# Optimization experiments

Hardware: AMD Instinct MI355X
Metric: run time of the kernel (lower is better)

The kernel has to match this reference:

```python
import jax, jax.numpy as jnp
import numpy as np

N = 50000
F_IN = 128
HID = 16
CLS = 40
NEG_SLOPE = 0.2


def gat_layer(x, src, dst, W, a_src, a_dst, b, heads, out_ch):
    # x: [N, Fin]; src/dst: [E] (self-loops included); W: [Fin, heads*out_ch]
    n = x.shape[0]
    h = (x @ W).reshape(n, heads, out_ch)                    # [N, H, C]
    al_s = jnp.einsum('nhc,hc->nh', h, a_src)                # [N, H]
    al_d = jnp.einsum('nhc,hc->nh', h, a_dst)                # [N, H]
    e = jax.nn.leaky_relu(al_s[src] + al_d[dst], NEG_SLOPE)  # [E, H]
    # segment softmax over incoming edges of each dst node
    m = jax.ops.segment_max(e, dst, num_segments=n)          # [N, H]
    ex = jnp.exp(e - m[dst])
    den = jax.ops.segment_sum(ex, dst, num_segments=n)
    alpha = ex / den[dst]                                    # [E, H]
    out = jax.ops.segment_sum(h[src] * alpha[:, :, None], dst, num_segments=n)
    return out.reshape(n, heads * out_ch) + b


def setup_inputs() -> dict:
    key = jax.random.key(0)
    ks = jax.random.split(key, 16)
    E = 800000
    x = jax.random.normal(ks[0], (N, F_IN), dtype=jnp.float32)
    edge_index = jax.random.randint(ks[1], (2, E), 0, N, dtype=jnp.int64)
    s = 0.1
    W1 = jax.random.normal(ks[2], (F_IN, 7 * HID), dtype=jnp.float32) * s
    a_src1 = jax.random.normal(ks[3], (7, HID), dtype=jnp.float32) * s
    a_dst1 = jax.random.normal(ks[4], (7, HID), dtype=jnp.float32) * s
    b1 = jnp.zeros((7 * HID,), dtype=jnp.float32)
    W2 = jax.random.normal(ks[5], (7 * HID, 6 * HID), dtype=jnp.float32) * s
    a_src2 = jax.random.normal(ks[6], (6, HID), dtype=jnp.float32) * s
    a_dst2 = jax.random.normal(ks[7], (6, HID), dtype=jnp.float32) * s
    b2 = jnp.zeros((6 * HID,), dtype=jnp.float32)
    W3 = jax.random.normal(ks[8], (6 * HID, 6 * CLS), dtype=jnp.float32) * s
    a_src3 = jax.random.normal(ks[9], (6, CLS), dtype=jnp.float32) * s
    a_dst3 = jax.random.normal(ks[10], (6, CLS), dtype=jnp.float32) * s
    b3 = jnp.zeros((6 * CLS,), dtype=jnp.float32)
    return {
        'x': x, 'edge_index': edge_index,
        'W1': W1, 'a_src1': a_src1, 'a_dst1': a_dst1, 'b1': b1,
        'W2': W2, 'a_src2': a_src2, 'a_dst2': a_dst2, 'b2': b2,
        'W3': W3, 'a_src3': a_src3, 'a_dst3': a_dst3, 'b3': b3,
    }


def reference(x, edge_index, W1, a_src1, a_dst1, b1, W2, a_src2, a_dst2, b2, W3, a_src3, a_dst3, b3):
    # add self-loops once (PyG GATConv default add_self_loops=True)
    loops = jnp.arange(N, dtype=edge_index.dtype)
    src = jnp.concatenate([edge_index[0], loops])
    dst = jnp.concatenate([edge_index[1], loops])
    # dropout layers are identity in eval mode
    h = gat_layer(x, src, dst, W1, a_src1, a_dst1, b1, 7, HID)
    h = jax.nn.relu(h)
    h = gat_layer(h, src, dst, W2, a_src2, a_dst2, b2, 6, HID)
    h = jax.nn.relu(h)
    out = gat_layer(h, src, dst, W3, a_src3, a_dst3, b3, 6, CLS)
    return out
```

## Files before the change

### kernel.cpp

```cpp
#include <hip/hip_runtime.h>
#include <hip/hip_fp16.h>
#include <cstdint>

#define NNODES 50000

__device__ inline void wave_lds_fence() {
  asm volatile("s_waitcnt lgkmcnt(0)" ::: "memory");
  __builtin_amdgcn_wave_barrier();
}

__global__ void hist_kernel(const int* __restrict__ ei, int E, int Nn, int* __restrict__ cnt) {
  int i = blockIdx.x * blockDim.x + threadIdx.x;
  int ET = E + Nn;
  if (i >= ET) return;
  int d = (i < E) ? ei[E + i] : (i - E);
  atomicAdd(&cnt[d], 1);
}

__global__ void scan1_kernel(const int* __restrict__ in, int n, int* __restrict__ incl,
                             int* __restrict__ bsum) {
  __shared__ int sd[256];
  int g = blockIdx.x * 256 + threadIdx.x;
  int v = (g < n) ? in[g] : 0;
  sd[threadIdx.x] = v;
  __syncthreads();
  for (int off = 1; off < 256; off <<= 1) {
    int t = (threadIdx.x >= off) ? sd[threadIdx.x - off] : 0;
    __syncthreads();
    sd[threadIdx.x] += t;
    __syncthreads();
  }
  if (g < n) incl[g] = sd[threadIdx.x];
  if (threadIdx.x == 255) bsum[blockIdx.x] = sd[255];
}

__global__ void scan3_kernel(const int* __restrict__ incl, const int* __restrict__ bscan,
                             int n, int* __restrict__ rowptr) {
  int g = blockIdx.x * 256 + threadIdx.x;
  if (g == 0) rowptr[0] = 0;
  if (g < n) {
    int off = (blockIdx.x > 0) ? bscan[blockIdx.x - 1] : 0;
    rowptr[g + 1] = incl[g] + off;
  }
}

__global__ void scatter_kernel(const int* __restrict__ ei, int E, int Nn,
                               const int* __restrict__ rowptr, int* __restrict__ cnt2,
                               int* __restrict__ esorted) {
  int i = blockIdx.x * blockDim.x + threadIdx.x;
  int ET = E + Nn;
  if (i >= ET) return;
  int s, d;
  if (i < E) { s = ei[i]; d = ei[E + i]; }
  else       { s = i - E; d = i - E; }
  int pos = rowptr[d] + atomicAdd(&cnt2[d], 1);
  esorted[pos] = s;
}

template <int FIN, int HC, int HCP, int BLOCK>
__global__ __launch_bounds__(BLOCK) void gemm_kernel(const float* __restrict__ X,
                                                     const float* __restrict__ W,
                                                     __half* __restrict__ Hout) {
  constexpr int NT = 16;
  constexpr int TM = 4, TN = 4;
  constexpr int CG = HC / TN;
  __shared__ __align__(16) float xs[FIN * NT];
  const int n0 = blockIdx.x * NT;
  for (int i = threadIdx.x * 4; i < NT * FIN; i += BLOCK * 4) {
    float4 v = *(const float4*)(X + (size_t)n0 * FIN + i);
    int node = i / FIN, k = i % FIN;
    xs[(k + 0) * NT + node] = v.x;
    xs[(k + 1) * NT + node] = v.y;
    xs[(k + 2) * NT + node] = v.z;
    xs[(k + 3) * NT + node] = v.w;
  }
  __syncthreads();
  const int cg = threadIdx.x % CG;
  const int ng = threadIdx.x / CG;
  if (ng >= NT / TM) return;
  const int c0 = cg * TN;
  const int i0 = ng * TM;
  float acc[TM][TN];
#pragma unroll
  for (int i = 0; i < TM; ++i)
#pragma unroll
    for (int j = 0; j < TN; ++j) acc[i][j] = 0.f;
#pragma unroll 4
  for (int k = 0; k < FIN; ++k) {
    const float4 wv = *(const float4*)(W + (size_t)k * HC + c0);
    const float4 xv = *(const float4*)(xs + k * NT + i0);
    acc[0][0] += xv.x * wv.x; acc[0][1] += xv.x * wv.y; acc[0][2] += xv.x * wv.z; acc[0][3] += xv.x * wv.w;
    acc[1][0] += xv.y * wv.x; acc[1][1] += xv.y * wv.y; acc[1][2] += xv.y * wv.z; acc[1][3] += xv.y * wv.w;
    acc[2][0] += xv.z * wv.x; acc[2][1] += xv.z * wv.y; acc[2][2] += xv.z * wv.z; acc[2][3] += xv.z * wv.w;
    acc[3][0] += xv.w * wv.x; acc[3][1] += xv.w * wv.y; acc[3][2] += xv.w * wv.z; acc[3][3] += xv.w * wv.w;
  }
#pragma unroll
  for (int i = 0; i < TM; ++i) {
    union { __half2 h2[2]; uint2 u; } pk;
    pk.h2[0] = __floats2half2_rn(acc[i][0], acc[i][1]);
    pk.h2[1] = __floats2half2_rn(acc[i][2], acc[i][3]);
    *(uint2*)(Hout + (size_t)(n0 + i0 + i) * HCP + c0) = pk.u;
  }
}

template <int H, int C, int HCP>
__global__ void alpha_kernel(const __half* __restrict__ Hbuf, const float* __restrict__ a_s,
                             const float* __restrict__ a_d, float* __restrict__ als8,
                             float* __restrict__ ald8, int n_nodes) {
  int i = blockIdx.x * blockDim.x + threadIdx.x;
  if (i >= n_nodes * H) return;
  int n = i / H, h = i % H;
  const __half2* hp = (const __half2*)(Hbuf + (size_t)n * HCP + (size_t)h * C);
  float s1 = 0.f, s2 = 0.f;
#pragma unroll
  for (int c = 0; c < C / 2; ++c) {
    float2 f = __half22float2(hp[c]);
    s1 += f.x * a_s[h * C + 2 * c] + f.y * a_s[h * C + 2 * c + 1];
    s2 += f.x * a_d[h * C + 2 * c] + f.y * a_d[h * C + 2 * c + 1];
  }
  als8[n * 8 + h] = s1;
  ald8[n * 8 + h] = s2;
}

template <int H, int C, int HCP, int RELU>
__global__ __launch_bounds__(256) void agg_kernel(const __half* __restrict__ Hbuf,
                                                  const float* __restrict__ als8,
                                                  const float* __restrict__ ald8,
                                                  const int* __restrict__ rowptr,
                                                  const int* __restrict__ esrc,
                                                  const float* __restrict__ bias,
                                                  float* __restrict__ Out, int n_nodes) {
  constexpr int HC = H * C;
  constexpr int NCHUNK = HC / 8;
  constexpr int GROUPS = (NCHUNK <= 16) ? 4 : 2;
  constexpr int LPG = 64 / GROUPS;
  constexpr int UN = 3;
  constexpr int TPAD = 72;
  const int wave = threadIdx.x >> 6;
  const int lane = threadIdx.x & 63;
  const int grp = lane / LPG;
  const int lg = lane % LPG;
  const int n = blockIdx.x * 4 + wave;
  __shared__ float s_w[4][TPAD * H];
  __shared__ int s_src[4][TPAD];
  if (n >= n_nodes) return;

  if (lane < TPAD - 64) s_src[wave][64 + lane] = 0;
  for (int z = lane; z < (TPAD - 64) * H; z += 64) s_w[wave][64 * H + z] = 0.f;

  const int e0 = rowptr[n];
  const int e1 = rowptr[n + 1];

  float aldn[H];
#pragma unroll
  for (int h = 0; h < H; ++h) aldn[h] = ald8[n * 8 + h];

  const int head = min((lg * 8) / C, H - 1);
  const bool act = lg < NCHUNK;

  float acc[8];
  float lsum = 0.f;
#pragma unroll
  for (int j = 0; j < 8; ++j) acc[j] = 0.f;

  for (int base = e0; base < e1; base += 64) {
    const int cnt = (e1 - base < 64) ? (e1 - base) : 64;
    int sreg = 0;
    if (lane < cnt) sreg = esrc[base + lane];
    s_src[wave][lane] = sreg;
    if (lane < cnt) {
      const float4 qa = *(const float4*)(als8 + (size_t)sreg * 8);
      const float4 qb = *(const float4*)(als8 + (size_t)sreg * 8 + 4);
      const float q[8] = {qa.x, qa.y, qa.z, qa.w, qb.x, qb.y, qb.z, qb.w};
#pragma unroll
      for (int h = 0; h < H; ++h) {
        float v = q[h] + aldn[h];
        v = v > 0.f ? v : 0.2f * v;
        s_w[wave][lane * H + h] = __expf(v);
      }
    } else {
#pragma unroll
      for (int h = 0; h < H; ++h) s_w[wave][lane * H + h] = 0.f;
    }
    wave_lds_fence();
    const int nit = (cnt + GROUPS - 1) / GROUPS;
    for (int i = 0; i < nit; i += UN) {
      int tt[UN], si[UN];
      uint4 v[UN];
      float w[UN];
#pragma unroll
      for (int k = 0; k < UN; ++k) tt[k] = (i + k) * GROUPS + grp;
#pragma unroll
      for (int k = 0; k < UN; ++k) si[k] = s_src[wave][tt[k]];
#pragma unroll
      for (int k = 0; k < UN; ++k)
        if (act) v[k] = *(const uint4*)(Hbuf + (size_t)si[k] * HCP + lg * 8);
#pragma unroll
      for (int k = 0; k < UN; ++k) w[k] = s_w[wave][tt[k] * H + head];
#pragma unroll
      for (int k = 0; k < UN; ++k)
        if (act) {
          const __half2* hp = (const __half2*)&v[k];
          float2 f0 = __half22float2(hp[0]);
          float2 f1 = __half22float2(hp[1]);
          float2 f2 = __half22float2(hp[2]);
          float2 f3 = __half22float2(hp[3]);
          lsum += w[k];
          acc[0] += w[k] * f0.x; acc[1] += w[k] * f0.y;
          acc[2] += w[k] * f1.x; acc[3] += w[k] * f1.y;
          acc[4] += w[k] * f2.x; acc[5] += w[k] * f2.y;
          acc[6] += w[k] * f3.x; acc[7] += w[k] * f3.y;
        }
    }
    wave_lds_fence();
  }

#pragma unroll
  for (int off = LPG; off < 64; off <<= 1) {
    lsum += __shfl_xor(lsum, off);
#pragma unroll
    for (int j = 0; j < 8; ++j) acc[j] += __shfl_xor(acc[j], off);
  }

  if (grp == 0 && act) {
    const float inv = 1.f / lsum;
    const float4 b0 = *(const float4*)(bias + lg * 8);
    const float4 b1 = *(const float4*)(bias + lg * 8 + 4);
    float4 o0, o1;
    o0.x = acc[0] * inv + b0.x; o0.y = acc[1] * inv + b0.y;
    o0.z = acc[2] * inv + b0.z; o0.w = acc[3] * inv + b0.w;
    o1.x = acc[4] * inv + b1.x; o1.y = acc[5] * inv + b1.y;
    o1.z = acc[6] * inv + b1.z; o1.w = acc[7] * inv + b1.w;
    if (RELU) {
      o0.x = fmaxf(o0.x, 0.f); o0.y = fmaxf(o0.y, 0.f);
      o0.z = fmaxf(o0.z, 0.f); o0.w = fmaxf(o0.w, 0.f);
      o1.x = fmaxf(o1.x, 0.f); o1.y = fmaxf(o1.y, 0.f);
      o1.z = fmaxf(o1.z, 0.f); o1.w = fmaxf(o1.w, 0.f);
    }
    *(float4*)(Out + (size_t)n * HC + lg * 8) = o0;
    *(float4*)(Out + (size_t)n * HC + lg * 8 + 4) = o1;
  }
}

extern "C" void kernel_launch(void* const* d_in, const int* in_sizes, int n_in,
                              void* d_out, int out_size, void* d_ws, size_t ws_size,
                              hipStream_t stream) {
  const int N = NNODES;
  const float* x  = (const float*)d_in[0];
  const int* ei   = (const int*)d_in[1];
  const float* W1 = (const float*)d_in[2];
  const float* as1 = (const float*)d_in[3];
  const float* ad1 = (const float*)d_in[4];
  const float* b1  = (const float*)d_in[5];
  const float* W2  = (const float*)d_in[6];
  const float* as2 = (const float*)d_in[7];
  const float* ad2 = (const float*)d_in[8];
  const float* b2  = (const float*)d_in[9];
  const float* W3  = (const float*)d_in[10];
  const float* as3 = (const float*)d_in[11];
  const float* ad3 = (const float*)d_in[12];
  const float* b3  = (const float*)d_in[13];
  float* out = (float*)d_out;
  const int E = in_sizes[1] / 2;
  const int ET = E + N;

  char* ws = (char*)d_ws;
  size_t off = 0;
  auto alloc = [&](size_t bytes) -> char* {
    char* p = ws + off;
    off += (bytes + 255) & ~(size_t)255;
    return p;
  };
  int* cnt     = (int*)alloc((size_t)N * 4);
  int* cnt2    = (int*)alloc((size_t)N * 4);
  int* incl    = (int*)alloc((size_t)N * 4);
  int* bsum    = (int*)alloc(512 * 4);
  int* bscan   = (int*)alloc(256 * 4);
  int* rowptr  = (int*)alloc((size_t)(N + 1) * 4);
  int* esorted = (int*)alloc((size_t)ET * 4);
  float* als   = (float*)alloc((size_t)N * 8 * 4);
  float* ald   = (float*)alloc((size_t)N * 8 * 4);
  __half* hbuf = (__half*)alloc((size_t)N * 256 * 2);
  float* abuf  = (float*)alloc((size_t)N * 112 * 4);

  hipMemsetAsync(cnt, 0, (size_t)N * 4, stream);
  hipMemsetAsync(cnt2, 0, (size_t)N * 4, stream);

  const int B1 = (N + 255) / 256;
  hist_kernel<<<(ET + 255) / 256, 256, 0, stream>>>(ei, E, N, cnt);
  scan1_kernel<<<B1, 256, 0, stream>>>(cnt, N, incl, bsum);
  scan1_kernel<<<1, 256, 0, stream>>>(bsum, B1, bscan, bsum + 256);
  scan3_kernel<<<B1, 256, 0, stream>>>(incl, bscan, N, rowptr);
  scatter_kernel<<<(ET + 255) / 256, 256, 0, stream>>>(ei, E, N, rowptr, cnt2, esorted);

  gemm_kernel<128, 112, 128, 128><<<N / 16, 128, 0, stream>>>(x, W1, hbuf);
  alpha_kernel<7, 16, 128><<<(N * 7 + 255) / 256, 256, 0, stream>>>(hbuf, as1, ad1, als, ald, N);
  agg_kernel<7, 16, 128, 1><<<(N + 3) / 4, 256, 0, stream>>>(hbuf, als, ald, rowptr, esorted, b1, abuf, N);
  gemm_kernel<112, 96, 96, 128><<<N / 16, 128, 0, stream>>>(abuf, W2, hbuf);
  alpha_kernel<6, 16, 96><<<(N * 6 + 255) / 256, 256, 0, stream>>>(hbuf, as2, ad2, als, ald, N);
  agg_kernel<6, 16, 96, 1><<<(N + 3) / 4, 256, 0, stream>>>(hbuf, als, ald, rowptr, esorted, b2, abuf, N);
  gemm_kernel<96, 240, 256, 256><<<N / 16, 256, 0, stream>>>(abuf, W3, hbuf);
  alpha_kernel<6, 40, 256><<<(N * 6 + 255) / 256, 256, 0, stream>>>(hbuf, as3, ad3, als, ald, N);
  agg_kernel<6, 40, 256, 0><<<(N + 3) / 4, 256, 0, stream>>>(hbuf, als, ald, rowptr, esorted, b3, out, N);
}
```

Baseline: 480.1 us.

## Partition edges by source range and aggregate per XCD-local range with combine pass

Edges are bucketed by destination and by one of four source-node ranges, using a finer-grained CSR built with a three-level scan. For layers 1 and 2, a partial aggregation kernel maps each source range to a pair of XCDs, so the gathered feature rows for that range stay resident in that XCD's L2. A combine kernel then sums the fp16 partials and softmax denominators and applies bias and ReLU. This trades an extra pass with partial-buffer writes and reads, fp16 rounding of partials, and a larger scan for better gather locality; layer 3 still uses the original aggregation.

After: 606.2 us. 26.3% more time.

```diff
diff --git a/kernel.cpp b/kernel.cpp
--- a/kernel.cpp
+++ b/kernel.cpp
@@ -3,6 +3,10 @@
 #include <cstdint>
 
 #define NNODES 50000
+#define RANGES 4
+#define RSPAN 12500
+
+typedef unsigned int nvec4 __attribute__((ext_vector_type(4)));
 
 __device__ inline void wave_lds_fence() {
   asm volatile("s_waitcnt lgkmcnt(0)" ::: "memory");
@@ -13,8 +17,10 @@
   int i = blockIdx.x * blockDim.x + threadIdx.x;
   int ET = E + Nn;
   if (i >= ET) return;
-  int d = (i < E) ? ei[E + i] : (i - E);
-  atomicAdd(&cnt[d], 1);
+  int s, d;
+  if (i < E) { s = ei[i]; d = ei[E + i]; }
+  else       { s = i - E; d = i - E; }
+  atomicAdd(&cnt[d * RANGES + s / RSPAN], 1);
 }
 
 __global__ void scan1_kernel(const int* __restrict__ in, int n, int* __restrict__ incl,
@@ -34,18 +40,25 @@
   if (threadIdx.x == 255) bsum[blockIdx.x] = sd[255];
 }
 
-__global__ void scan3_kernel(const int* __restrict__ incl, const int* __restrict__ bscan,
-                             int n, int* __restrict__ rowptr) {
+__global__ void scan3seg_kernel(const int* __restrict__ incl0, const int* __restrict__ incl1,
+                                const int* __restrict__ incl2, int n, int* __restrict__ segptr) {
   int g = blockIdx.x * 256 + threadIdx.x;
-  if (g == 0) rowptr[0] = 0;
+  if (g == 0) segptr[0] = 0;
   if (g < n) {
-    int off = (blockIdx.x > 0) ? bscan[blockIdx.x - 1] : 0;
-    rowptr[g + 1] = incl[g] + off;
+    int b0 = g >> 8;
+    int off = 0;
+    if (b0 > 0) {
+      int i = b0 - 1;
+      off = incl1[i];
+      int j = i >> 8;
+      if (j > 0) off += incl2[j - 1];
+    }
+    segptr[g + 1] = incl0[g] + off;
   }
 }
 
 __global__ void scatter_kernel(const int* __restrict__ ei, int E, int Nn,
-                               const int* __restrict__ rowptr, int* __restrict__ cnt2,
+                               const int* __restrict__ segptr, int* __restrict__ cnt2,
                                int* __restrict__ esorted) {
   int i = blockIdx.x * blockDim.x + threadIdx.x;
   int ET = E + Nn;
@@ -53,7 +66,8 @@
   int s, d;
   if (i < E) { s = ei[i]; d = ei[E + i]; }
   else       { s = i - E; d = i - E; }
-  int pos = rowptr[d] + atomicAdd(&cnt2[d], 1);
+  int seg = d * RANGES + s / RSPAN;
+  int pos = segptr[seg] + atomicAdd(&cnt2[seg], 1);
   esorted[pos] = s;
 }
 
@@ -126,7 +140,7 @@
 __global__ __launch_bounds__(256) void agg_kernel(const __half* __restrict__ Hbuf,
                                                   const float* __restrict__ als8,
                                                   const float* __restrict__ ald8,
-                                                  const int* __restrict__ rowptr,
+                                                  const int* __restrict__ segptr,
                                                   const int* __restrict__ esrc,
                                                   const float* __restrict__ bias,
                                                   float* __restrict__ Out, int n_nodes) {
@@ -148,8 +162,8 @@
   if (lane < TPAD - 64) s_src[wave][64 + lane] = 0;
   for (int z = lane; z < (TPAD - 64) * H; z += 64) s_w[wave][64 * H + z] = 0.f;
 
-  const int e0 = rowptr[n];
-  const int e1 = rowptr[n + 1];
+  const int e0 = segptr[n * RANGES];
+  const int e1 = segptr[n * RANGES + RANGES];
 
   float aldn[H];
 #pragma unroll
@@ -240,6 +254,166 @@
     *(float4*)(Out + (size_t)n * HC + lg * 8) = o0;
     *(float4*)(Out + (size_t)n * HC + lg * 8 + 4) = o1;
   }
+}
+
+template <int H, int C, int HCP>
+__global__ __launch_bounds__(256) void agg_part_kernel(const __half* __restrict__ Hbuf,
+                                                       const float* __restrict__ als8,
+                                                       const float* __restrict__ ald8,
+                                                       const int* __restrict__ segptr,
+                                                       const int* __restrict__ esrc,
+                                                       __half* __restrict__ Ppart,
+                                                       float* __restrict__ Plsum) {
+  constexpr int HC = H * C;
+  constexpr int NCHUNK = HC / 8;
+  constexpr int GROUPS = 4;
+  constexpr int LPG = 16;
+  constexpr int UN = 3;
+  constexpr int TPAD = 72;
+  const int wave = threadIdx.x >> 6;
+  const int lane = threadIdx.x & 63;
+  const int grp = lane / LPG;
+  const int lg = lane % LPG;
+  const int xcd = blockIdx.x & 7;
+  const int r = xcd >> 1;
+  const int half = xcd & 1;
+  const int nb = blockIdx.x >> 3;
+  const int n = (nb * 2 + half) * 4 + wave;
+  __shared__ float s_w[4][TPAD * H];
+  __shared__ int s_src[4][TPAD];
+
+  if (lane < TPAD - 64) s_src[wave][64 + lane] = 0;
+  for (int z = lane; z < (TPAD - 64) * H; z += 64) s_w[wave][64 * H + z] = 0.f;
+
+  const int e0 = segptr[n * RANGES + r];
+  const int e1 = segptr[n * RANGES + r + 1];
+
+  float aldn[H];
+#pragma unroll
+  for (int h = 0; h < H; ++h) aldn[h] = ald8[n * 8 + h];
+
+  const int head = min((lg * 8) / C, H - 1);
+  const bool act = lg < NCHUNK;
+
+  float acc[8];
+  float lsum = 0.f;
+#pragma unroll
+  for (int j = 0; j < 8; ++j) acc[j] = 0.f;
+
+  for (int base = e0; base < e1; base += 64) {
+    const int cnt = (e1 - base < 64) ? (e1 - base) : 64;
+    int sreg = 0;
+    if (lane < cnt) sreg = esrc[base + lane];
+    s_src[wave][lane] = sreg;
+    if (lane < cnt) {
+      const float4 qa = *(const float4*)(als8 + (size_t)sreg * 8);
+      const float4 qb = *(const float4*)(als8 + (size_t)sreg * 8 + 4);
+      const float q[8] = {qa.x, qa.y, qa.z, qa.w, qb.x, qb.y, qb.z, qb.w};
+#pragma unroll
+      for (int h = 0; h < H; ++h) {
+        float v = q[h] + aldn[h];
+        v = v > 0.f ? v : 0.2f * v;
+        s_w[wave][lane * H + h] = __expf(v);
+      }
+    } else {
+#pragma unroll
+      for (int h = 0; h < H; ++h) s_w[wave][lane * H + h] = 0.f;
+    }
+    wave_lds_fence();
+    const int nit = (cnt + GROUPS - 1) / GROUPS;
+    for (int i = 0; i < nit; i += UN) {
+      int tt[UN], si[UN];
+      uint4 v[UN];
+      float w[UN];
+#pragma unroll
+      for (int k = 0; k < UN; ++k) tt[k] = (i + k) * GROUPS + grp;
+#pragma unroll
+      for (int k = 0; k < UN; ++k) si[k] = s_src[wave][tt[k]];
+#pragma unroll
+      for (int k = 0; k < UN; ++k)
+        if (act) v[k] = *(const uint4*)(Hbuf + (size_t)si[k] * HCP + lg * 8);
+#pragma unroll
+      for (int k = 0; k < UN; ++k) w[k] = s_w[wave][tt[k] * H + head];
+#pragma unroll
+      for (int k = 0; k < UN; ++k)
+        if (act) {
+          const __half2* hp = (const __half2*)&v[k];
+          float2 f0 = __half22float2(hp[0]);
+          float2 f1 = __half22float2(hp[1]);
+          float2 f2 = __half22float2(hp[2]);
+          float2 f3 = __half22float2(hp[3]);
+          lsum += w[k];
+          acc[0] += w[k] * f0.x; acc[1] += w[k] * f0.y;
+          acc[2] += w[k] * f1.x; acc[3] += w[k] * f1.y;
+          acc[4] += w[k] * f2.x; acc[5] += w[k] * f2.y;
+          acc[6] += w[k] * f3.x; acc[7] += w[k] * f3.y;
+        }
+    }
+    wave_lds_fence();
+  }
+
+#pragma unroll
+  for (int off = LPG; off < 64; off <<= 1) {
+    lsum += __shfl_xor(lsum, off);
+#pragma unroll
+    for (int j = 0; j < 8; ++j) acc[j] += __shfl_xor(acc[j], off);
+  }
+
+  if (grp == 0 && act) {
+    union { __half2 h2[4]; nvec4 u; } pk;
+    pk.h2[0] = __floats2half2_rn(acc[0], acc[1]);
+    pk.h2[1] = __floats2half2_rn(acc[2], acc[3]);
+    pk.h2[2] = __floats2half2_rn(acc[4], acc[5]);
+    pk.h2[3] = __floats2half2_rn(acc[6], acc[7]);
+    __builtin_nontemporal_store(pk.u, (nvec4*)(Ppart + ((size_t)r * NNODES + n) * HC + lg * 8));
+    if ((lg * 8) % C == 0)
+      __builtin_nontemporal_store(lsum, Plsum + ((size_t)r * NNODES + n) * 8 + head);
+  }
+}
+
+template <int H, int C, int RELU>
+__global__ __launch_bounds__(256) void combine_kernel(const __half* __restrict__ Ppart,
+                                                      const float* __restrict__ Plsum,
+                                                      const float* __restrict__ bias,
+                                                      float* __restrict__ Out, int n_nodes) {
+  constexpr int HC = H * C;
+  constexpr int NCH = HC / 8;
+  int t = blockIdx.x * 256 + threadIdx.x;
+  if (t >= n_nodes * NCH) return;
+  int n = t / NCH, ck = t % NCH;
+  int head = (ck * 8) / C;
+  float ls = 0.f;
+  float a[8];
+#pragma unroll
+  for (int j = 0; j < 8; ++j) a[j] = 0.f;
+#pragma unroll
+  for (int r = 0; r < RANGES; ++r) {
+    ls += Plsum[((size_t)r * NNODES + n) * 8 + head];
+    uint4 u = *(const uint4*)(Ppart + ((size_t)r * NNODES + n) * HC + ck * 8);
+    const __half2* hp = (const __half2*)&u;
+#pragma unroll
+    for (int p = 0; p < 4; ++p) {
+      float2 f = __half22float2(hp[p]);
+      a[2 * p] += f.x;
+      a[2 * p + 1] += f.y;
+    }
+  }
+  const float inv = 1.f / ls;
+  const float4 b0 = *(const float4*)(bias + ck * 8);
+  const float4 b1 = *(const float4*)(bias + ck * 8 + 4);
+  float4 o0, o1;
+  o0.x = a[0] * inv + b0.x; o0.y = a[1] * inv + b0.y;
+  o0.z = a[2] * inv + b0.z; o0.w = a[3] * inv + b0.w;
+  o1.x = a[4] * inv + b1.x; o1.y = a[5] * inv + b1.y;
+  o1.z = a[6] * inv + b1.z; o1.w = a[7] * inv + b1.w;
+  if (RELU) {
+    o0.x = fmaxf(o0.x, 0.f); o0.y = fmaxf(o0.y, 0.f);
+    o0.z = fmaxf(o0.z, 0.f); o0.w = fmaxf(o0.w, 0.f);
+    o1.x = fmaxf(o1.x, 0.f); o1.y = fmaxf(o1.y, 0.f);
+    o1.z = fmaxf(o1.z, 0.f); o1.w = fmaxf(o1.w, 0.f);
+  }
+  *(float4*)(Out + (size_t)n * HC + ck * 8) = o0;
+  *(float4*)(Out + (size_t)n * HC + ck * 8 + 4) = o1;
 }
 
 extern "C" void kernel_launch(void* const* d_in, const int* in_sizes, int n_in,
@@ -263,6 +437,7 @@
   float* out = (float*)d_out;
   const int E = in_sizes[1] / 2;
   const int ET = E + N;
+  const int NSEG = N * RANGES;
 
   char* ws = (char*)d_ws;
   size_t off = 0;
@@ -271,35 +446,52 @@
     off += (bytes + 255) & ~(size_t)255;
     return p;
   };
-  int* cnt     = (int*)alloc((size_t)N * 4);
-  int* cnt2    = (int*)alloc((size_t)N * 4);
-  int* incl    = (int*)alloc((size_t)N * 4);
-  int* bsum    = (int*)alloc(512 * 4);
-  int* bscan   = (int*)alloc(256 * 4);
-  int* rowptr  = (int*)alloc((size_t)(N + 1) * 4);
+  int* cnt     = (int*)alloc((size_t)NSEG * 4);
+  int* cnt2    = (int*)alloc((size_t)NSEG * 4);
+  int* incl0   = (int*)alloc((size_t)NSEG * 4);
+  int* bs0     = (int*)alloc(1024 * 4);
+  int* incl1   = (int*)alloc(1024 * 4);
+  int* bs1     = (int*)alloc(256 * 4);
+  int* incl2   = (int*)alloc(256 * 4);
+  int* bs2     = (int*)alloc(256 * 4);
+  int* segptr  = (int*)alloc((size_t)(NSEG + 1) * 4);
   int* esorted = (int*)alloc((size_t)ET * 4);
   float* als   = (float*)alloc((size_t)N * 8 * 4);
   float* ald   = (float*)alloc((size_t)N * 8 * 4);
   __half* hbuf = (__half*)alloc((size_t)N * 256 * 2);
   float* abuf  = (float*)alloc((size_t)N * 112 * 4);
-
-  hipMemsetAsync(cnt, 0, (size_t)N * 4, stream);
-  hipMemsetAsync(cnt2, 0, (size_t)N * 4, stream);
-
-  const int B1 = (N + 255) / 256;
+  __half* ppart = (__half*)alloc((size_t)RANGES * N * 112 * 2);
+  float* plsum  = (float*)alloc((size_t)RANGES * N * 8 * 4);
+  const bool use_part = (off <= ws_size);
+
+  hipMemsetAsync(cnt, 0, (size_t)NSEG * 4, stream);
+  hipMemsetAsync(cnt2, 0, (size_t)NSEG * 4, stream);
+
+  const int BSEG = (NSEG + 255) / 256;
   hist_kernel<<<(ET + 255) / 256, 256, 0, stream>>>(ei, E, N, cnt);
-  scan1_kernel<<<B1, 256, 0, stream>>>(cnt, N, incl, bsum);
-  scan1_kernel<<<1, 256, 0, stream>>>(bsum, B1, bscan, bsum + 256);
-  scan3_kernel<<<B1, 256, 0, stream>>>(incl, bscan, N, rowptr);
-  scatter_kernel<<<(ET + 255) / 256, 256, 0, stream>>>(ei, E, N, rowptr, cnt2, esorted);
+  scan1_kernel<<<BSEG, 256, 0, stream>>>(cnt, NSEG, incl0, bs0);
+  scan1_kernel<<<(BSEG + 255) / 256, 256, 0, stream>>>(bs0, BSEG, incl1, bs1);
+  scan1_kernel<<<1, 256, 0, stream>>>(bs1, (BSEG + 255) / 256, incl2, bs2);
+  scan3seg_kernel<<<BSEG, 256, 0, stream>>>(incl0, incl1, incl2, NSEG, segptr);
+  scatter_kernel<<<(ET + 255) / 256, 256, 0, stream>>>(ei, E, N, segptr, cnt2, esorted);
 
   gemm_kernel<128, 112, 128, 128><<<N / 16, 128, 0, stream>>>(x, W1, hbuf);
   alpha_kernel<7, 16, 128><<<(N * 7 + 255) / 256, 256, 0, stream>>>(hbuf, as1, ad1, als, ald, N);
-  agg_kernel<7, 16, 128, 1><<<(N + 3) / 4, 256, 0, stream>>>(hbuf, als, ald, rowptr, esorted, b1, abuf, N);
+  if (use_part) {
+    agg_part_kernel<7, 16, 128><<<(N / 8) * 8, 256, 0, stream>>>(hbuf, als, ald, segptr, esorted, ppart, plsum);
+    combine_kernel<7, 16, 1><<<(N * 14 + 255) / 256, 256, 0, stream>>>(ppart, plsum, b1, abuf, N);
+  } else {
+    agg_kernel<7, 16, 128, 1><<<(N + 3) / 4, 256, 0, stream>>>(hbuf, als, ald, segptr, esorted, b1, abuf, N);
+  }
   gemm_kernel<112, 96, 96, 128><<<N / 16, 128, 0, stream>>>(abuf, W2, hbuf);
   alpha_kernel<6, 16, 96><<<(N * 6 + 255) / 256, 256, 0, stream>>>(hbuf, as2, ad2, als, ald, N);
-  agg_kernel<6, 16, 96, 1><<<(N + 3) / 4, 256, 0, stream>>>(hbuf, als, ald, rowptr, esorted, b2, abuf, N);
+  if (use_part) {
+    agg_part_kernel<6, 16, 96><<<(N / 8) * 8, 256, 0, stream>>>(hbuf, als, ald, segptr, esorted, ppart, plsum);
+    combine_kernel<6, 16, 1><<<(N * 12 + 255) / 256, 256, 0, stream>>>(ppart, plsum, b2, abuf, N);
+  } else {
+    agg_kernel<6, 16, 96, 1><<<(N + 3) / 4, 256, 0, stream>>>(hbuf, als, ald, segptr, esorted, b2, abuf, N);
+  }
   gemm_kernel<96, 240, 256, 256><<<N / 16, 256, 0, stream>>>(abuf, W3, hbuf);
   alpha_kernel<6, 40, 256><<<(N * 6 + 255) / 256, 256, 0, stream>>>(hbuf, as3, ad3, als, ald, N);
-  agg_kernel<6, 40, 256, 0><<<(N + 3) / 4, 256, 0, stream>>>(hbuf, als, ald, rowptr, esorted, b3, out, N);
-}
+  agg_kernel<6, 40, 256, 0><<<(N + 3) / 4, 256, 0, stream>>>(hbuf, als, ald, segptr, esorted, b3, out, N);
+}
```
